# Kernel tuning notes

Measured on AMD Instinct MI355X. Metric: run time of the kernel, lower is better.

Reference implementation:

```python
import jax, jax.numpy as jnp
import numpy as np

NUM_CLASSES = 10
WEIGHT = tuple([0.1] * NUM_CLASSES)
EXPONENT = 2


def setup_inputs() -> dict:
    key = jax.random.key(0)
    k1, k2, k3 = jax.random.split(key, 3)
    B, Y, X = 64, 512, 512
    outputs = jax.random.normal(k1, (B, Y, X), dtype=jnp.float32)
    # targets hold integer intensity classes 0..9 stored as floats (original does float subtraction)
    targets = jax.random.randint(k2, (B, Y, X), 0, NUM_CLASSES).astype(jnp.float32)
    # observation-station mask: 1 where a station exists, 0 elsewhere
    mask = jax.random.randint(k3, (B, Y, X), 0, 2).astype(jnp.int32)
    return {"outputs": outputs, "targets": targets, "mask": mask}


def reference(outputs, targets, mask):
    # Class id per pixel; invalid (mask==0) pixels routed to dummy segment NUM_CLASSES.
    cls = targets.astype(jnp.int32)
    valid = mask == 1
    ids = jnp.where(valid, cls, NUM_CLASSES).ravel()  # [B*Y*X]

    sqerr = (outputs - targets) ** EXPONENT  # [B,Y,X]
    # One fused scatter-reduce replaces the original triple Python loop over 10 masks.
    per_class_sum = jax.ops.segment_sum(sqerr.ravel(), ids, num_segments=NUM_CLASSES + 1)[:NUM_CLASSES]
    class_n = jax.ops.segment_sum(jnp.ones_like(sqerr).ravel(), ids, num_segments=NUM_CLASSES + 1)[:NUM_CLASSES]

    loss_each = jnp.where(class_n > 0, per_class_sum / jnp.maximum(class_n, 1.0), 0.0)  # [10]
    weight = jnp.asarray(WEIGHT, dtype=outputs.dtype)
    loss = jnp.sum(weight * loss_each)
    return loss, loss_each, class_n
```

## Files before the change

kernel.cpp:

```cpp
#include <hip/hip_runtime.h>

#define NCLS 10
#define ACC_STRIDE 64


__global__ __launch_bounds__(256) void loss_main_kernel(
    const float* __restrict__ outputs,
    const float* __restrict__ targets,
    const int*   __restrict__ mask,
    float* __restrict__ ws,
    int n4)
{
    float sum[NCLS];
    float cnt[NCLS];
#pragma unroll
    for (int c = 0; c < NCLS; ++c) { sum[c] = 0.0f; cnt[c] = 0.0f; }

    const float4* o4 = (const float4*)outputs;
    const float4* t4 = (const float4*)targets;
    const int4*   m4 = (const int4*)mask;

    int tid    = blockIdx.x * blockDim.x + threadIdx.x;
    int stride = gridDim.x * blockDim.x;

    for (int i = tid; i < n4; i += stride) {
        float4 o = o4[i];
        float4 t = t4[i];
        int4   m = m4[i];

        float od[4] = {o.x, o.y, o.z, o.w};
        float td[4] = {t.x, t.y, t.z, t.w};
        int   md[4] = {m.x, m.y, m.z, m.w};

#pragma unroll
        for (int j = 0; j < 4; ++j) {
            float d  = od[j] - td[j];
            float sq = d * d;
            int cls = (md[j] == 1) ? (int)td[j] : NCLS;
#pragma unroll
            for (int c = 0; c < NCLS; ++c) {
                float match = (cls == c) ? 1.0f : 0.0f;
                cnt[c] += match;
                sum[c] = fmaf(match, sq, sum[c]);
            }
        }
    }

#pragma unroll
    for (int c = 0; c < NCLS; ++c) {
#pragma unroll
        for (int off = 32; off > 0; off >>= 1) {
            sum[c] += __shfl_down(sum[c], off, 64);
            cnt[c] += __shfl_down(cnt[c], off, 64);
        }
    }

    __shared__ float ls[4][2 * NCLS];
    int wave = threadIdx.x >> 6;
    int lane = threadIdx.x & 63;
    if (lane == 0) {
#pragma unroll
        for (int c = 0; c < NCLS; ++c) {
            ls[wave][c]        = sum[c];
            ls[wave][NCLS + c] = cnt[c];
        }
    }
    __syncthreads();

    if (threadIdx.x < 2 * NCLS) {
        float v = ls[0][threadIdx.x] + ls[1][threadIdx.x]
                + ls[2][threadIdx.x] + ls[3][threadIdx.x];
        atomicAdd(&ws[threadIdx.x * ACC_STRIDE], v);
    }
}

__global__ __launch_bounds__(64) void loss_final_kernel(
    const float* __restrict__ ws,
    float* __restrict__ out)
{
    int lane = threadIdx.x;
    float le = 0.0f;
    if (lane < NCLS) {
        float s  = ws[lane * ACC_STRIDE];
        float cn = ws[(NCLS + lane) * ACC_STRIDE];
        le = (cn > 0.0f) ? (s / fmaxf(cn, 1.0f)) : 0.0f;
        out[1 + lane]  = le;
        out[11 + lane] = cn;
    }
    float w = 0.1f * le;
#pragma unroll
    for (int off = 32; off > 0; off >>= 1) w += __shfl_down(w, off, 64);
    if (lane == 0) out[0] = w;
}

extern "C" void kernel_launch(void* const* d_in, const int* in_sizes, int n_in,
                              void* d_out, int out_size, void* d_ws, size_t ws_size,
                              hipStream_t stream)
{
    const float* outputs = (const float*)d_in[0];
    const float* targets = (const float*)d_in[1];
    const int*   mask    = (const int*)d_in[2];
    float* out = (float*)d_out;
    float* ws  = (float*)d_ws;

    int n  = in_sizes[0];
    int n4 = n / 4;

    hipMemsetAsync(d_ws, 0, 2 * NCLS * ACC_STRIDE * sizeof(float), stream);

    loss_main_kernel<<<1024, 256, 0, stream>>>(outputs, targets, mask, ws, n4);
    loss_final_kernel<<<1, 64, 0, stream>>>(ws, out);
}
```

Measured before the change: 199.7 us.

## Replace register one-hot class accumulation with per-thread LDS histogram atomics

Each thread now accumulates squared error and counts into its own column of a shared-memory histogram via LDS atomicAdd indexed by class, instead of updating all ten register accumulators per element. This removes the per-element loop over every class. The main loop is split into full strides unrolled by four plus a tail, and the block reduction sums histogram rows per wave. It adds about 22KB of shared memory per block, which can reduce occupancy, and it relies on LDS atomic throughput.

```diff
diff --git a/kernel.cpp b/kernel.cpp
--- a/kernel.cpp
+++ b/kernel.cpp
@@ -1,76 +1,102 @@
 #include <hip/hip_runtime.h>
 
-#define NCLS 10
+#define NCLS  10
+#define NSLOT 11
+#define TPB   256
+#define NBLK  1024
 #define ACC_STRIDE 64
 
 
-__global__ __launch_bounds__(256) void loss_main_kernel(
+__global__ __launch_bounds__(TPB) void loss_main_kernel(
     const float* __restrict__ outputs,
     const float* __restrict__ targets,
     const int*   __restrict__ mask,
     float* __restrict__ ws,
     int n4)
 {
-    float sum[NCLS];
-    float cnt[NCLS];
-#pragma unroll
-    for (int c = 0; c < NCLS; ++c) { sum[c] = 0.0f; cnt[c] = 0.0f; }
+    __shared__ float hist[2 * NSLOT * TPB];
+
+    for (int k = threadIdx.x; k < 2 * NSLOT * TPB; k += TPB)
+        hist[k] = 0.0f;
+    __syncthreads();
 
     const float4* o4 = (const float4*)outputs;
     const float4* t4 = (const float4*)targets;
     const int4*   m4 = (const int4*)mask;
 
-    int tid    = blockIdx.x * blockDim.x + threadIdx.x;
-    int stride = gridDim.x * blockDim.x;
+    const int tid = blockIdx.x * TPB + threadIdx.x;
+    const int T   = NBLK * TPB;
+    const int full = n4 / T;
+    const int tx = threadIdx.x;
 
-    for (int i = tid; i < n4; i += stride) {
+#pragma unroll 4
+    for (int r = 0; r < full; ++r) {
+        int i = tid + r * T;
         float4 o = o4[i];
         float4 t = t4[i];
         int4   m = m4[i];
 
-        float od[4] = {o.x, o.y, o.z, o.w};
-        float td[4] = {t.x, t.y, t.z, t.w};
-        int   md[4] = {m.x, m.y, m.z, m.w};
-
-#pragma unroll
-        for (int j = 0; j < 4; ++j) {
-            float d  = od[j] - td[j];
-            float sq = d * d;
-            int cls = (md[j] == 1) ? (int)td[j] : NCLS;
-#pragma unroll
-            for (int c = 0; c < NCLS; ++c) {
-                float match = (cls == c) ? 1.0f : 0.0f;
-                cnt[c] += match;
-                sum[c] = fmaf(match, sq, sum[c]);
-            }
+        {
+            float d = o.x - t.x; float sq = d * d;
+            int cls = (m.x == 1) ? (int)t.x : NCLS;
+            int idx = cls * TPB + tx;
+            atomicAdd(&hist[idx], sq);
+            atomicAdd(&hist[NSLOT * TPB + idx], 1.0f);
+        }
+        {
+            float d = o.y - t.y; float sq = d * d;
+            int cls = (m.y == 1) ? (int)t.y : NCLS;
+            int idx = cls * TPB + tx;
+            atomicAdd(&hist[idx], sq);
+            atomicAdd(&hist[NSLOT * TPB + idx], 1.0f);
+        }
+        {
+            float d = o.z - t.z; float sq = d * d;
+            int cls = (m.z == 1) ? (int)t.z : NCLS;
+            int idx = cls * TPB + tx;
+            atomicAdd(&hist[idx], sq);
+            atomicAdd(&hist[NSLOT * TPB + idx], 1.0f);
+        }
+        {
+            float d = o.w - t.w; float sq = d * d;
+            int cls = (m.w == 1) ? (int)t.w : NCLS;
+            int idx = cls * TPB + tx;
+            atomicAdd(&hist[idx], sq);
+            atomicAdd(&hist[NSLOT * TPB + idx], 1.0f);
         }
     }
-
-#pragma unroll
-    for (int c = 0; c < NCLS; ++c) {
-#pragma unroll
-        for (int off = 32; off > 0; off >>= 1) {
-            sum[c] += __shfl_down(sum[c], off, 64);
-            cnt[c] += __shfl_down(cnt[c], off, 64);
-        }
+    for (int i = tid + full * T; i < n4; i += T) {
+        float4 o = o4[i];
+        float4 t = t4[i];
+        int4   m = m4[i];
+        float dx = o.x - t.x, dy = o.y - t.y, dz = o.z - t.z, dw = o.w - t.w;
+        int cx = (m.x == 1) ? (int)t.x : NCLS;
+        int cy = (m.y == 1) ? (int)t.y : NCLS;
+        int cz = (m.z == 1) ? (int)t.z : NCLS;
+        int cw = (m.w == 1) ? (int)t.w : NCLS;
+        atomicAdd(&hist[cx * TPB + tx], dx * dx);
+        atomicAdd(&hist[NSLOT * TPB + cx * TPB + tx], 1.0f);
+        atomicAdd(&hist[cy * TPB + tx], dy * dy);
+        atomicAdd(&hist[NSLOT * TPB + cy * TPB + tx], 1.0f);
+        atomicAdd(&hist[cz * TPB + tx], dz * dz);
+        atomicAdd(&hist[NSLOT * TPB + cz * TPB + tx], 1.0f);
+        atomicAdd(&hist[cw * TPB + tx], dw * dw);
+        atomicAdd(&hist[NSLOT * TPB + cw * TPB + tx], 1.0f);
     }
 
-    __shared__ float ls[4][2 * NCLS];
-    int wave = threadIdx.x >> 6;
-    int lane = threadIdx.x & 63;
-    if (lane == 0) {
-#pragma unroll
-        for (int c = 0; c < NCLS; ++c) {
-            ls[wave][c]        = sum[c];
-            ls[wave][NCLS + c] = cnt[c];
-        }
-    }
     __syncthreads();
 
-    if (threadIdx.x < 2 * NCLS) {
-        float v = ls[0][threadIdx.x] + ls[1][threadIdx.x]
-                + ls[2][threadIdx.x] + ls[3][threadIdx.x];
-        atomicAdd(&ws[threadIdx.x * ACC_STRIDE], v);
+    int wave = tx >> 6;
+    int lane = tx & 63;
+    for (int j = wave; j < 2 * NCLS; j += 4) {
+        const float* src = (j < NCLS) ? &hist[j * TPB]
+                                      : &hist[NSLOT * TPB + (j - NCLS) * TPB];
+        float v = src[lane] + src[lane + 64] + src[lane + 128] + src[lane + 192];
+#pragma unroll
+        for (int off = 32; off > 0; off >>= 1)
+            v += __shfl_down(v, off, 64);
+        if (lane == 0)
+            atomicAdd(&ws[j * ACC_STRIDE], v);
     }
 }
 
@@ -107,7 +133,6 @@
     int n4 = n / 4;
 
     hipMemsetAsync(d_ws, 0, 2 * NCLS * ACC_STRIDE * sizeof(float), stream);
-
-    loss_main_kernel<<<1024, 256, 0, stream>>>(outputs, targets, mask, ws, n4);
+    loss_main_kernel<<<NBLK, TPB, 0, stream>>>(outputs, targets, mask, ws, n4);
     loss_final_kernel<<<1, 64, 0, stream>>>(ws, out);
 }
```

Result: slower. 301.9 us (+51.2%).

## Pack per-class counts into 6-bit fields and double-buffer nontemporal loads

Applied to the files above, without the earlier changes.

Replaces the ten float per-class counters with a single 64-bit integer holding 6-bit fields, so each element does one shift-add instead of ten float adds. It also software-pipelines two vector loads per thread with nontemporal loads, doubles the grid to 2048 blocks, and adds scalar tail handling. The aim is to cut VALU work in a loop that appears compute-bound. The packed counters only stay correct while each thread handles fewer than 64 elements, which ties correctness to the input size and grid.

```diff
diff --git a/kernel.cpp b/kernel.cpp
--- a/kernel.cpp
+++ b/kernel.cpp
@@ -1,75 +1,129 @@
 #include <hip/hip_runtime.h>
 
 #define NCLS 10
+#define TPB  256
+#define NBLK 2048
 #define ACC_STRIDE 64
 
+typedef float vfloat4 __attribute__((ext_vector_type(4)));
+typedef int   vint4   __attribute__((ext_vector_type(4)));
 
-__global__ __launch_bounds__(256) void loss_main_kernel(
+
+__device__ __forceinline__ void proc_elem(float o, float t, int m,
+                                          float sum[NCLS], unsigned long long &cnt)
+{
+    float d  = o - t;
+    float sq = d * d;
+    int cls  = (m == 1) ? (int)t : NCLS;
+    cnt += 1ull << (6 * cls);
+#pragma unroll
+    for (int c = 0; c < NCLS; ++c)
+        sum[c] += (cls == c) ? sq : 0.0f;
+}
+
+__global__ __launch_bounds__(TPB) void loss_main_kernel(
     const float* __restrict__ outputs,
     const float* __restrict__ targets,
     const int*   __restrict__ mask,
     float* __restrict__ ws,
-    int n4)
+    int n4, int n_rem_base, int n_rem)
 {
+    const vfloat4* o4 = (const vfloat4*)outputs;
+    const vfloat4* t4 = (const vfloat4*)targets;
+    const vint4*   m4 = (const vint4*)mask;
+
+    const int tid = blockIdx.x * TPB + threadIdx.x;
+    const int T   = NBLK * TPB;
+
     float sum[NCLS];
-    float cnt[NCLS];
 #pragma unroll
-    for (int c = 0; c < NCLS; ++c) { sum[c] = 0.0f; cnt[c] = 0.0f; }
+    for (int c = 0; c < NCLS; ++c) sum[c] = 0.0f;
+    unsigned long long cnt = 0;
 
-    const float4* o4 = (const float4*)outputs;
-    const float4* t4 = (const float4*)targets;
-    const int4*   m4 = (const int4*)mask;
+    const int full  = n4 / T;
+    const int kfull = full & ~1;
 
-    int tid    = blockIdx.x * blockDim.x + threadIdx.x;
-    int stride = gridDim.x * blockDim.x;
+    if (kfull >= 2) {
+        vfloat4 oA = __builtin_nontemporal_load(&o4[tid]);
+        vfloat4 tA = __builtin_nontemporal_load(&t4[tid]);
+        vint4   mA = __builtin_nontemporal_load(&m4[tid]);
+        vfloat4 oB = __builtin_nontemporal_load(&o4[tid + T]);
+        vfloat4 tB = __builtin_nontemporal_load(&t4[tid + T]);
+        vint4   mB = __builtin_nontemporal_load(&m4[tid + T]);
 
-    for (int i = tid; i < n4; i += stride) {
-        float4 o = o4[i];
-        float4 t = t4[i];
-        int4   m = m4[i];
-
-        float od[4] = {o.x, o.y, o.z, o.w};
-        float td[4] = {t.x, t.y, t.z, t.w};
-        int   md[4] = {m.x, m.y, m.z, m.w};
-
-#pragma unroll
-        for (int j = 0; j < 4; ++j) {
-            float d  = od[j] - td[j];
-            float sq = d * d;
-            int cls = (md[j] == 1) ? (int)td[j] : NCLS;
-#pragma unroll
-            for (int c = 0; c < NCLS; ++c) {
-                float match = (cls == c) ? 1.0f : 0.0f;
-                cnt[c] += match;
-                sum[c] = fmaf(match, sq, sum[c]);
+        int k = 0;
+        while (true) {
+            proc_elem(oA.x, tA.x, mA.x, sum, cnt);
+            proc_elem(oA.y, tA.y, mA.y, sum, cnt);
+            proc_elem(oA.z, tA.z, mA.z, sum, cnt);
+            proc_elem(oA.w, tA.w, mA.w, sum, cnt);
+            if (k + 2 < kfull) {
+                int i = tid + (k + 2) * T;
+                oA = __builtin_nontemporal_load(&o4[i]);
+                tA = __builtin_nontemporal_load(&t4[i]);
+                mA = __builtin_nontemporal_load(&m4[i]);
             }
+            proc_elem(oB.x, tB.x, mB.x, sum, cnt);
+            proc_elem(oB.y, tB.y, mB.y, sum, cnt);
+            proc_elem(oB.z, tB.z, mB.z, sum, cnt);
+            proc_elem(oB.w, tB.w, mB.w, sum, cnt);
+            if (k + 3 < kfull) {
+                int i = tid + (k + 3) * T;
+                oB = __builtin_nontemporal_load(&o4[i]);
+                tB = __builtin_nontemporal_load(&t4[i]);
+                mB = __builtin_nontemporal_load(&m4[i]);
+            }
+            k += 2;
+            if (k >= kfull) break;
         }
     }
+    for (int i = tid + kfull * T; i < n4; i += T) {
+        vfloat4 o = __builtin_nontemporal_load(&o4[i]);
+        vfloat4 t = __builtin_nontemporal_load(&t4[i]);
+        vint4   m = __builtin_nontemporal_load(&m4[i]);
+        proc_elem(o.x, t.x, m.x, sum, cnt);
+        proc_elem(o.y, t.y, m.y, sum, cnt);
+        proc_elem(o.z, t.z, m.z, sum, cnt);
+        proc_elem(o.w, t.w, m.w, sum, cnt);
+    }
+    if (tid < n_rem)
+        proc_elem(outputs[n_rem_base + tid], targets[n_rem_base + tid],
+                  mask[n_rem_base + tid], sum, cnt);
+
+    float cfl[NCLS];
+#pragma unroll
+    for (int c = 0; c < NCLS; ++c)
+        cfl[c] = (float)((unsigned)(cnt >> (6 * c)) & 63u);
 
 #pragma unroll
     for (int c = 0; c < NCLS; ++c) {
 #pragma unroll
         for (int off = 32; off > 0; off >>= 1) {
             sum[c] += __shfl_down(sum[c], off, 64);
-            cnt[c] += __shfl_down(cnt[c], off, 64);
+            cfl[c] += __shfl_down(cfl[c], off, 64);
         }
     }
 
-    __shared__ float ls[4][2 * NCLS];
+    __shared__ float lsS[4][NCLS];
+    __shared__ float lsC[4][NCLS];
     int wave = threadIdx.x >> 6;
     int lane = threadIdx.x & 63;
     if (lane == 0) {
 #pragma unroll
         for (int c = 0; c < NCLS; ++c) {
-            ls[wave][c]        = sum[c];
-            ls[wave][NCLS + c] = cnt[c];
+            lsS[wave][c] = sum[c];
+            lsC[wave][c] = cfl[c];
         }
     }
     __syncthreads();
 
     if (threadIdx.x < 2 * NCLS) {
-        float v = ls[0][threadIdx.x] + ls[1][threadIdx.x]
-                + ls[2][threadIdx.x] + ls[3][threadIdx.x];
+        int c = (threadIdx.x < NCLS) ? threadIdx.x : (threadIdx.x - NCLS);
+        float v;
+        if (threadIdx.x < NCLS)
+            v = lsS[0][c] + lsS[1][c] + lsS[2][c] + lsS[3][c];
+        else
+            v = lsC[0][c] + lsC[1][c] + lsC[2][c] + lsC[3][c];
         atomicAdd(&ws[threadIdx.x * ACC_STRIDE], v);
     }
 }
@@ -105,9 +159,11 @@
 
     int n  = in_sizes[0];
     int n4 = n / 4;
+    int n_rem_base = 4 * n4;
+    int n_rem = n - n_rem_base;
 
     hipMemsetAsync(d_ws, 0, 2 * NCLS * ACC_STRIDE * sizeof(float), stream);
-
-    loss_main_kernel<<<1024, 256, 0, stream>>>(outputs, targets, mask, ws, n4);
+    loss_main_kernel<<<NBLK, TPB, 0, stream>>>(outputs, targets, mask, ws,
+                                               n4, n_rem_base, n_rem);
     loss_final_kernel<<<1, 64, 0, stream>>>(ws, out);
 }
```

Measured after the change: 193.7 us. 3.0% less time.
